# Kernel tuning notes

Measured on AMD Instinct MI355X. Metric: run time of the kernel, lower is better.

The kernel has to match this reference:

```python
import jax, jax.numpy as jnp
import numpy as np
from math import factorial, sqrt

BATCH = 4096
RS_IN = [(16, 0), (16, 1), (16, 2)]   # (mul, l), parity 0
RS_OUT = [(16, 0), (16, 1), (16, 2)]

# selection rule: l_filter in [|l_in-l_out|, l_in+l_out]
SET_LF = sorted({l for (_, li) in RS_IN for (_, lo) in RS_OUT
                 for l in range(abs(li - lo), li + lo + 1)})
Y_OFF = {l: sum(2 * k + 1 for k in SET_LF if k < l) for l in SET_LF}
Y_DIM = sum(2 * l + 1 for l in SET_LF)  # 25


def wigner_3j(j1, j2, j3, m1, m2, m3):
    if m1 + m2 + m3 != 0 or not (abs(j1 - j2) <= j3 <= j1 + j2):
        return 0.0
    if abs(m1) > j1 or abs(m2) > j2 or abs(m3) > j3:
        return 0.0
    f = factorial
    pre = sqrt(f(j1 + j2 - j3) * f(j1 - j2 + j3) * f(-j1 + j2 + j3) / f(j1 + j2 + j3 + 1))
    pre *= sqrt(f(j1 + m1) * f(j1 - m1) * f(j2 + m2) * f(j2 - m2) * f(j3 + m3) * f(j3 - m3))
    s = 0.0
    for t in range(max(0, j2 - j3 - m1, j1 - j3 + m2),
                   min(j1 + j2 - j3, j1 - m1, j2 + m2) + 1):
        s += (-1) ** t / (f(t) * f(j3 - j2 + m1 + t) * f(j3 - j1 - m2 + t)
                          * f(j1 + j2 - j3 - t) * f(j1 - m1 - t) * f(j2 + m2 - t))
    return (-1) ** (j1 - j2 - m3) * pre * s


def real_to_complex(l):
    # A[M+l, m+l]: complex Y^M expressed in the real SH basis
    A = np.zeros((2 * l + 1, 2 * l + 1), dtype=np.complex128)
    A[l, l] = 1.0
    s2 = 1.0 / np.sqrt(2.0)
    for m in range(1, l + 1):
        A[l + m, l + m] = (-1) ** m * s2
        A[l + m, l - m] = 1j * (-1) ** m * s2
        A[l - m, l + m] = s2
        A[l - m, l - m] = -1j * s2
    return A


def clebsch_gordan(l1, l2, l3):
    # real, unit-Frobenius-norm invariant 3-tensor (unique up to sign)
    T = np.zeros((2 * l1 + 1, 2 * l2 + 1, 2 * l3 + 1))
    for m1 in range(-l1, l1 + 1):
        for m2 in range(-l2, l2 + 1):
            m3 = -(m1 + m2)
            if abs(m3) <= l3:
                T[m1 + l1, m2 + l2, m3 + l3] = wigner_3j(l1, l2, l3, m1, m2, m3)
    A1, A2, A3 = real_to_complex(l1), real_to_complex(l2), real_to_complex(l3)
    C = np.einsum('abc,ai,bj,ck->ijk', T, A1.conj(), A2.conj(), A3.conj())
    C = C.real if np.linalg.norm(C.real) >= np.linalg.norm(C.imag) else C.imag
    n = np.linalg.norm(C)
    return (C / n).astype(np.float32) if n > 0 else C.astype(np.float32)


# precompute per-block padded CG tensors and R offsets
R_OFF = {}
C_BLOCKS = {}
_off = 0
for _i, (_mo, _lo) in enumerate(RS_OUT):
    for _j, (_mi, _li) in enumerate(RS_IN):
        _lfs = list(range(abs(_li - _lo), _li + _lo + 1))
        R_OFF[(_i, _j)] = (_off, len(_lfs))
        _off += _mo * _mi * len(_lfs)
        _C = np.zeros((len(_lfs), 2 * _lo + 1, 2 * _li + 1, Y_DIM), dtype=np.float32)
        for _k, _lf in enumerate(_lfs):
            _o = Y_OFF[_lf]
            _C[_k, :, :, _o:_o + 2 * _lf + 1] = clebsch_gordan(_lo, _li, _lf)
        C_BLOCKS[(_i, _j)] = jnp.asarray(_C)
N_PATH = _off  # 4864


def setup_inputs() -> dict:
    key = jax.random.key(0)
    k1, k2, k3 = jax.random.split(key, 3)
    Y = jax.random.normal(k1, (Y_DIM, BATCH), dtype=jnp.float32)
    R = jax.random.normal(k2, (BATCH, N_PATH), dtype=jnp.float32)
    norm_coef = jax.random.uniform(k3, (len(RS_OUT), len(RS_IN), BATCH),
                                   dtype=jnp.float32, minval=0.5, maxval=1.5)
    return {"Y": Y, "R": R, "norm_coef": norm_coef}


def reference(Y, R, norm_coef):
    # Y: [Y_DIM, batch], R: [batch, N_PATH], norm_coef: [3, 3, batch]
    batch = Y.shape[1]
    rows = []
    for i, (mo, lo) in enumerate(RS_OUT):
        row = []
        for j, (mi, li) in enumerate(RS_IN):
            off, nlf = R_OFF[(i, j)]
            sub_R = R[:, off:off + mo * mi * nlf].reshape(batch, mo, mi, nlf)
            # fuse the per-l_filter loop into one contraction over k and m
            K = jnp.einsum('kijm,mz,zuvk,z->zuivj',
                           C_BLOCKS[(i, j)], Y, sub_R, norm_coef[i, j])
            row.append(K.reshape(batch, mo * (2 * lo + 1), mi * (2 * li + 1)))
        rows.append(jnp.concatenate(row, axis=2))
    return jnp.concatenate(rows, axis=1)  # [batch, 144, 144]
```

## Files before the change

kernel.cpp:

```cpp
#include <hip/hip_runtime.h>

#define NPATH 4864
#define YDIM  25
#define NW    259
#define NCG   1225

__device__ float g_cg[NCG];
__device__ int   g_wtab[NW * 2];

__device__ __forceinline__ double dfact(int n) {
    double f = 1.0;
    for (int i = 2; i <= n; ++i) f *= (double)i;
    return f;
}
__device__ __forceinline__ int iabs_(int x) { return x < 0 ? -x : x; }
__device__ __forceinline__ int imax3(int a, int b, int c) { int m = a > b ? a : b; return m > c ? m : c; }
__device__ __forceinline__ int imin3(int a, int b, int c) { int m = a < b ? a : b; return m < c ? m : c; }

__device__ double wig3j(int j1, int j2, int j3, int m1, int m2, int m3) {
    if (m1 + m2 + m3 != 0) return 0.0;
    if (iabs_(m1) > j1 || iabs_(m2) > j2 || iabs_(m3) > j3) return 0.0;
    if (j3 < iabs_(j1 - j2) || j3 > j1 + j2) return 0.0;
    double pre = sqrt(dfact(j1 + j2 - j3) * dfact(j1 - j2 + j3) * dfact(-j1 + j2 + j3)
                      / dfact(j1 + j2 + j3 + 1));
    pre *= sqrt(dfact(j1 + m1) * dfact(j1 - m1) * dfact(j2 + m2) * dfact(j2 - m2)
                * dfact(j3 + m3) * dfact(j3 - m3));
    int t0 = imax3(0, j2 - j3 - m1, j1 - j3 + m2);
    int t1 = imin3(j1 + j2 - j3, j1 - m1, j2 + m2);
    double s = 0.0;
    for (int t = t0; t <= t1; ++t) {
        double d = dfact(t) * dfact(j3 - j2 + m1 + t) * dfact(j3 - j1 - m2 + t)
                 * dfact(j1 + j2 - j3 - t) * dfact(j1 - m1 - t) * dfact(j2 + m2 - t);
        s += ((t & 1) ? -1.0 : 1.0) / d;
    }
    int p = j1 - j2 - m3;
    p = ((p % 2) + 2) % 2;
    return (p ? -1.0 : 1.0) * pre * s;
}

__device__ void fill_A(int l, double* Are, double* Aim) {
    int n = 2 * l + 1;
    for (int i = 0; i < n * n; ++i) { Are[i] = 0.0; Aim[i] = 0.0; }
    Are[l * n + l] = 1.0;
    double s2 = sqrt(0.5);
    for (int m = 1; m <= l; ++m) {
        double sgn = (m & 1) ? -1.0 : 1.0;
        Are[(l + m) * n + (l + m)] = sgn * s2;
        Aim[(l + m) * n + (l - m)] = sgn * s2;
        Are[(l - m) * n + (l + m)] = s2;
        Aim[(l - m) * n + (l - m)] = -s2;
    }
}

__global__ __launch_bounds__(64) void setup_kernel() {
    const int CL1[19]  = {0,0,0,1,1,1,1,1,1,1,2,2,2,2,2,2,2,2,2};
    const int CL2[19]  = {0,1,2,0,1,1,1,2,2,2,0,1,1,1,2,2,2,2,2};
    const int CL3[19]  = {0,1,2,1,0,1,2,1,2,3,2,1,2,3,0,1,2,3,4};
    const int COFF[19] = {0,1,10,35,44,53,80,125,170,245,350,375,420,495,600,625,700,825,1000};

    int c = blockIdx.x;
    int t = threadIdx.x;

    if (c == 0 && t == 63) {
        const int NLFt[9]   = {1,1,1,1,3,3,1,3,5};
        const int CGOFF9[9] = {0,1,10,35,44,125,350,375,600};
        int w = 0;
        for (int ij = 0; ij < 9; ++ij) {
            int lo = ij / 3, li = ij % 3;
            int lfmin = lo > li ? lo - li : li - lo;
            int no2 = 2 * lo + 1, ni2 = 2 * li + 1;
            int cgo = CGOFF9[ij];
            for (int k = 0; k < NLFt[ij]; ++k) {
                int lf = lfmin + k;
                for (int a = 0; a < no2; ++a)
                    for (int b = 0; b < ni2; ++b) {
                        g_wtab[2 * w]     = cgo + (a * ni2 + b) * (2 * lf + 1);
                        g_wtab[2 * w + 1] = lf;
                        ++w;
                    }
                cgo += no2 * ni2 * (2 * lf + 1);
            }
        }
    }

    int l1 = CL1[c], l2 = CL2[c], l3 = CL3[c], coff = COFF[c];
    int n1 = 2 * l1 + 1, n2 = 2 * l2 + 1, n3 = 2 * l3 + 1;

    __shared__ double A1re[25], A1im[25], A2re[25], A2im[25], A3re[81], A3im[81];
    __shared__ double Tm[25];
    __shared__ double Cre[225], Cim[225];
    __shared__ double redR[64], redI[64];

    if (t == 0)      fill_A(l1, A1re, A1im);
    else if (t == 1) fill_A(l2, A2re, A2im);
    else if (t == 2) fill_A(l3, A3re, A3im);
    else if (t == 3) {
        for (int a = 0; a < n1; ++a)
            for (int b = 0; b < n2; ++b) {
                int m1 = a - l1, m2 = b - l2, m3 = -(m1 + m2);
                Tm[a * n2 + b] = (iabs_(m3) <= l3) ? wig3j(l1, l2, l3, m1, m2, m3) : 0.0;
            }
    }
    __syncthreads();

    int ntot = n1 * n2 * n3;
    double sre = 0.0, sim = 0.0;
    for (int idx = t; idx < ntot; idx += 64) {
        int i3 = idx % n3;
        int r  = idx / n3;
        int i2 = r % n2;
        int i1 = r / n2;
        double ar = 0.0, ai = 0.0;
        for (int a = 0; a < n1; ++a) {
            double x1r = A1re[a * n1 + i1], x1i = -A1im[a * n1 + i1];
            for (int b = 0; b < n2; ++b) {
                double tv = Tm[a * n2 + b];
                if (tv == 0.0) continue;
                int m3 = -((a - l1) + (b - l2));
                if (iabs_(m3) > l3) continue;
                double x2r = A2re[b * n2 + i2], x2i = -A2im[b * n2 + i2];
                double x3r = A3re[(m3 + l3) * n3 + i3], x3i = -A3im[(m3 + l3) * n3 + i3];
                double pr = x1r * x2r - x1i * x2i;
                double pi = x1r * x2i + x1i * x2r;
                double qr = pr * x3r - pi * x3i;
                double qi = pr * x3i + pi * x3r;
                ar += tv * qr;
                ai += tv * qi;
            }
        }
        Cre[idx] = ar; Cim[idx] = ai;
        sre += ar * ar; sim += ai * ai;
    }
    redR[t] = sre; redI[t] = sim;
    __syncthreads();
    if (t == 0) {
        double a = 0.0, b = 0.0;
        for (int q = 0; q < 64; ++q) { a += redR[q]; b += redI[q]; }
        redR[0] = a; redI[0] = b;
    }
    __syncthreads();
    double totR = redR[0], totI = redI[0];
    bool useRe = (totR >= totI);
    double nn  = sqrt(useRe ? totR : totI);
    double inv = (nn > 0.0) ? 1.0 / nn : 0.0;
    for (int idx = t; idx < ntot; idx += 64)
        g_cg[coff + idx] = (float)((useRe ? Cre[idx] : Cim[idx]) * inv);
}

template <int LO, int LI, int NLF_>
__device__ __forceinline__ void do_block(const float* __restrict__ Wl,
                                         const float* __restrict__ Rl,
                                         float nrm, float* __restrict__ outcol,
                                         int v, int b, int woff, int roff, int rowbase) {
    constexpr int NO2 = 2 * LO + 1, NI2 = 2 * LI + 1;
    float Wreg[NLF_ * NO2];
#pragma unroll
    for (int k = 0; k < NLF_; ++k)
#pragma unroll
        for (int a = 0; a < NO2; ++a)
            Wreg[k * NO2 + a] = Wl[woff + (k * NO2 + a) * NI2 + b];
#pragma unroll 4
    for (int u = 0; u < 16; ++u) {
        int rb = roff + (u * 16 + v) * NLF_;
        float Rk[NLF_];
#pragma unroll
        for (int k = 0; k < NLF_; ++k) Rk[k] = Rl[rb + k];
        float* orow = outcol + (rowbase + u * NO2) * 144;
#pragma unroll
        for (int a = 0; a < NO2; ++a) {
            float acc = 0.f;
#pragma unroll
            for (int k = 0; k < NLF_; ++k) acc += Wreg[k * NO2 + a] * Rk[k];
            orow[a * 144] = nrm * acc;
        }
    }
}

__global__ __launch_bounds__(256) void tp_kernel(const float* __restrict__ Yg,
                                                 const float* __restrict__ Rg,
                                                 const float* __restrict__ Ng,
                                                 float* __restrict__ Og, int batch) {
    __shared__ __align__(16) float Rl[NPATH];
    __shared__ float Wl[NW];
    __shared__ float Ys[YDIM];

    int z = blockIdx.x;
    int t = threadIdx.x;

    const float4* Rg4 = (const float4*)(Rg + (size_t)z * NPATH);
    float4* Rl4 = (float4*)Rl;
    for (int p = t; p < NPATH / 4; p += 256) Rl4[p] = Rg4[p];
    if (t < YDIM) Ys[t] = Yg[t * batch + z];
    __syncthreads();

    for (int w = t; w < NW; w += 256) {
        int off = g_wtab[2 * w], lf = g_wtab[2 * w + 1];
        float acc = 0.f;
        for (int ci = 0; ci <= 2 * lf; ++ci) acc += g_cg[off + ci] * Ys[lf * lf + ci];
        Wl[w] = acc;
    }
    __syncthreads();

    if (t >= 144) return;

    int j, v, b;
    if (t < 16)      { j = 0; v = t; b = 0; }
    else if (t < 64) { int q = t - 16; j = 1; v = q / 3; b = q - 3 * v; }
    else             { int q = t - 64; j = 2; v = q / 5; b = q - 5 * v; }

    float* outcol = Og + (size_t)z * 20736 + t;
    float n0 = Ng[(0 * 3 + j) * batch + z];
    float n1 = Ng[(1 * 3 + j) * batch + z];
    float n2 = Ng[(2 * 3 + j) * batch + z];

    if (j == 0) {
        do_block<0, 0, 1>(Wl, Rl, n0, outcol, v, b,   0,    0,  0);
        do_block<1, 0, 1>(Wl, Rl, n1, outcol, v, b,   9,  768, 16);
        do_block<2, 0, 1>(Wl, Rl, n2, outcol, v, b,  84, 2560, 64);
    } else if (j == 1) {
        do_block<0, 1, 1>(Wl, Rl, n0, outcol, v, b,   1,  256,  0);
        do_block<1, 1, 3>(Wl, Rl, n1, outcol, v, b,  12, 1024, 16);
        do_block<2, 1, 3>(Wl, Rl, n2, outcol, v, b,  89, 2816, 64);
    } else {
        do_block<0, 2, 1>(Wl, Rl, n0, outcol, v, b,   4,  512,  0);
        do_block<1, 2, 3>(Wl, Rl, n1, outcol, v, b,  39, 1792, 16);
        do_block<2, 2, 5>(Wl, Rl, n2, outcol, v, b, 134, 3584, 64);
    }
}

extern "C" void kernel_launch(void* const* d_in, const int* in_sizes, int n_in,
                              void* d_out, int out_size, void* d_ws, size_t ws_size,
                              hipStream_t stream) {
    const float* Y = (const float*)d_in[0];
    const float* R = (const float*)d_in[1];
    const float* N = (const float*)d_in[2];
    float* O = (float*)d_out;
    int batch = in_sizes[0] / YDIM;

    hipLaunchKernelGGL(setup_kernel, dim3(19), dim3(64), 0, stream);
    hipLaunchKernelGGL(tp_kernel, dim3(batch), dim3(256), 0, stream, Y, R, N, O, batch);
}
```

Baseline: 474.2 us.

## Precompute CG tables at compile time and align thread-to-column mapping to wavefronts

Moves Clebsch-Gordan coefficient and weight-offset table generation from a runtime setup kernel into constexpr evaluation stored in constant memory, which removes one kernel launch per call. It also remaps threads so each input-l group (j) starts on a 64-thread wavefront boundary, which avoids divergent branches inside a wavefront across the three do_block paths. The cost is more idle threads per block and reads from constant memory with non-uniform indices in the W computation.

```diff
diff --git a/kernel.cpp b/kernel.cpp
--- a/kernel.cpp
+++ b/kernel.cpp
@@ -5,147 +5,130 @@
 #define NW    259
 #define NCG   1225
 
-__device__ float g_cg[NCG];
-__device__ int   g_wtab[NW * 2];
-
-__device__ __forceinline__ double dfact(int n) {
-    double f = 1.0;
-    for (int i = 2; i <= n; ++i) f *= (double)i;
-    return f;
-}
-__device__ __forceinline__ int iabs_(int x) { return x < 0 ? -x : x; }
-__device__ __forceinline__ int imax3(int a, int b, int c) { int m = a > b ? a : b; return m > c ? m : c; }
-__device__ __forceinline__ int imin3(int a, int b, int c) { int m = a < b ? a : b; return m < c ? m : c; }
-
-__device__ double wig3j(int j1, int j2, int j3, int m1, int m2, int m3) {
+
+struct Tables {
+    float cg[NCG];
+    int   woff[NW];
+    int   wlf[NW];
+};
+
+constexpr double cfact(int n) { double f = 1.0; for (int i = 2; i <= n; ++i) f *= (double)i; return f; }
+
+constexpr double csqrt_(double x) {
+    if (x <= 0.0) return 0.0;
+    double g = x > 1.0 ? x : 1.0, p = 0.0;
+    for (int it = 0; it < 200; ++it) { p = g; g = 0.5 * (g + x / g); if (g == p) break; }
+    return g;
+}
+constexpr int cabs_(int x) { return x < 0 ? -x : x; }
+constexpr int cmax3(int a, int b, int c) { int m = a > b ? a : b; return m > c ? m : c; }
+constexpr int cmin3(int a, int b, int c) { int m = a < b ? a : b; return m < c ? m : c; }
+
+constexpr double cwig3j(int j1, int j2, int j3, int m1, int m2, int m3) {
     if (m1 + m2 + m3 != 0) return 0.0;
-    if (iabs_(m1) > j1 || iabs_(m2) > j2 || iabs_(m3) > j3) return 0.0;
-    if (j3 < iabs_(j1 - j2) || j3 > j1 + j2) return 0.0;
-    double pre = sqrt(dfact(j1 + j2 - j3) * dfact(j1 - j2 + j3) * dfact(-j1 + j2 + j3)
-                      / dfact(j1 + j2 + j3 + 1));
-    pre *= sqrt(dfact(j1 + m1) * dfact(j1 - m1) * dfact(j2 + m2) * dfact(j2 - m2)
-                * dfact(j3 + m3) * dfact(j3 - m3));
-    int t0 = imax3(0, j2 - j3 - m1, j1 - j3 + m2);
-    int t1 = imin3(j1 + j2 - j3, j1 - m1, j2 + m2);
+    if (cabs_(m1) > j1 || cabs_(m2) > j2 || cabs_(m3) > j3) return 0.0;
+    if (j3 < cabs_(j1 - j2) || j3 > j1 + j2) return 0.0;
+    double prod = cfact(j1 + j2 - j3) * cfact(j1 - j2 + j3) * cfact(-j1 + j2 + j3)
+                / cfact(j1 + j2 + j3 + 1);
+    prod *= cfact(j1 + m1) * cfact(j1 - m1) * cfact(j2 + m2) * cfact(j2 - m2)
+          * cfact(j3 + m3) * cfact(j3 - m3);
+    double pre = csqrt_(prod);
+    int t0 = cmax3(0, j2 - j3 - m1, j1 - j3 + m2);
+    int t1 = cmin3(j1 + j2 - j3, j1 - m1, j2 + m2);
     double s = 0.0;
     for (int t = t0; t <= t1; ++t) {
-        double d = dfact(t) * dfact(j3 - j2 + m1 + t) * dfact(j3 - j1 - m2 + t)
-                 * dfact(j1 + j2 - j3 - t) * dfact(j1 - m1 - t) * dfact(j2 + m2 - t);
+        double d = cfact(t) * cfact(j3 - j2 + m1 + t) * cfact(j3 - j1 - m2 + t)
+                 * cfact(j1 + j2 - j3 - t) * cfact(j1 - m1 - t) * cfact(j2 + m2 - t);
         s += ((t & 1) ? -1.0 : 1.0) / d;
     }
-    int p = j1 - j2 - m3;
-    p = ((p % 2) + 2) % 2;
+    int p = j1 - j2 - m3; p = ((p % 2) + 2) % 2;
     return (p ? -1.0 : 1.0) * pre * s;
 }
 
-__device__ void fill_A(int l, double* Are, double* Aim) {
-    int n = 2 * l + 1;
-    for (int i = 0; i < n * n; ++i) { Are[i] = 0.0; Aim[i] = 0.0; }
-    Are[l * n + l] = 1.0;
-    double s2 = sqrt(0.5);
-    for (int m = 1; m <= l; ++m) {
+struct Ent { int col; double re; double im; };
+
+constexpr int arow(int l, int a, Ent* e) {
+    int m = a - l;
+    double s2 = csqrt_(0.5);
+    if (m == 0) { e[0] = Ent{l, 1.0, 0.0}; return 1; }
+    if (m > 0) {
         double sgn = (m & 1) ? -1.0 : 1.0;
-        Are[(l + m) * n + (l + m)] = sgn * s2;
-        Aim[(l + m) * n + (l - m)] = sgn * s2;
-        Are[(l - m) * n + (l + m)] = s2;
-        Aim[(l - m) * n + (l - m)] = -s2;
-    }
-}
-
-__global__ __launch_bounds__(64) void setup_kernel() {
+        e[0] = Ent{l + m, sgn * s2, 0.0};
+        e[1] = Ent{l - m, 0.0, sgn * s2};
+        return 2;
+    }
+    int mm = -m;
+    e[0] = Ent{l + mm, s2, 0.0};
+    e[1] = Ent{l - mm, 0.0, -s2};
+    return 2;
+}
+
+constexpr Tables make_tables() {
+    Tables T{};
     const int CL1[19]  = {0,0,0,1,1,1,1,1,1,1,2,2,2,2,2,2,2,2,2};
     const int CL2[19]  = {0,1,2,0,1,1,1,2,2,2,0,1,1,1,2,2,2,2,2};
     const int CL3[19]  = {0,1,2,1,0,1,2,1,2,3,2,1,2,3,0,1,2,3,4};
     const int COFF[19] = {0,1,10,35,44,53,80,125,170,245,350,375,420,495,600,625,700,825,1000};
 
-    int c = blockIdx.x;
-    int t = threadIdx.x;
-
-    if (c == 0 && t == 63) {
-        const int NLFt[9]   = {1,1,1,1,3,3,1,3,5};
-        const int CGOFF9[9] = {0,1,10,35,44,125,350,375,600};
-        int w = 0;
-        for (int ij = 0; ij < 9; ++ij) {
-            int lo = ij / 3, li = ij % 3;
-            int lfmin = lo > li ? lo - li : li - lo;
-            int no2 = 2 * lo + 1, ni2 = 2 * li + 1;
-            int cgo = CGOFF9[ij];
-            for (int k = 0; k < NLFt[ij]; ++k) {
-                int lf = lfmin + k;
-                for (int a = 0; a < no2; ++a)
-                    for (int b = 0; b < ni2; ++b) {
-                        g_wtab[2 * w]     = cgo + (a * ni2 + b) * (2 * lf + 1);
-                        g_wtab[2 * w + 1] = lf;
-                        ++w;
-                    }
-                cgo += no2 * ni2 * (2 * lf + 1);
-            }
-        }
-    }
-
-    int l1 = CL1[c], l2 = CL2[c], l3 = CL3[c], coff = COFF[c];
-    int n1 = 2 * l1 + 1, n2 = 2 * l2 + 1, n3 = 2 * l3 + 1;
-
-    __shared__ double A1re[25], A1im[25], A2re[25], A2im[25], A3re[81], A3im[81];
-    __shared__ double Tm[25];
-    __shared__ double Cre[225], Cim[225];
-    __shared__ double redR[64], redI[64];
-
-    if (t == 0)      fill_A(l1, A1re, A1im);
-    else if (t == 1) fill_A(l2, A2re, A2im);
-    else if (t == 2) fill_A(l3, A3re, A3im);
-    else if (t == 3) {
+    for (int c = 0; c < 19; ++c) {
+        int l1 = CL1[c], l2 = CL2[c], l3 = CL3[c], coff = COFF[c];
+        int n1 = 2 * l1 + 1, n2 = 2 * l2 + 1, n3 = 2 * l3 + 1, ntot = n1 * n2 * n3;
+        double Cre[225] = {}, Cim[225] = {};
         for (int a = 0; a < n1; ++a)
             for (int b = 0; b < n2; ++b) {
                 int m1 = a - l1, m2 = b - l2, m3 = -(m1 + m2);
-                Tm[a * n2 + b] = (iabs_(m3) <= l3) ? wig3j(l1, l2, l3, m1, m2, m3) : 0.0;
+                if (cabs_(m3) > l3) continue;
+                double tv = cwig3j(l1, l2, l3, m1, m2, m3);
+                if (tv == 0.0) continue;
+                int crow = m3 + l3;
+                Ent e1[2] = {}, e2[2] = {}, e3[2] = {};
+                int k1 = arow(l1, a, e1), k2 = arow(l2, b, e2), k3 = arow(l3, crow, e3);
+                for (int x = 0; x < k1; ++x)
+                    for (int y = 0; y < k2; ++y)
+                        for (int w = 0; w < k3; ++w) {
+                            double r1 = e1[x].re, i1 = -e1[x].im;
+                            double r2 = e2[y].re, i2 = -e2[y].im;
+                            double r3 = e3[w].re, i3 = -e3[w].im;
+                            double pr = r1 * r2 - i1 * i2, pi = r1 * i2 + i1 * r2;
+                            double qr = pr * r3 - pi * i3, qi = pr * i3 + pi * r3;
+                            int idx = (e1[x].col * n2 + e2[y].col) * n3 + e3[w].col;
+                            Cre[idx] += tv * qr;
+                            Cim[idx] += tv * qi;
+                        }
             }
-    }
-    __syncthreads();
-
-    int ntot = n1 * n2 * n3;
-    double sre = 0.0, sim = 0.0;
-    for (int idx = t; idx < ntot; idx += 64) {
-        int i3 = idx % n3;
-        int r  = idx / n3;
-        int i2 = r % n2;
-        int i1 = r / n2;
-        double ar = 0.0, ai = 0.0;
-        for (int a = 0; a < n1; ++a) {
-            double x1r = A1re[a * n1 + i1], x1i = -A1im[a * n1 + i1];
-            for (int b = 0; b < n2; ++b) {
-                double tv = Tm[a * n2 + b];
-                if (tv == 0.0) continue;
-                int m3 = -((a - l1) + (b - l2));
-                if (iabs_(m3) > l3) continue;
-                double x2r = A2re[b * n2 + i2], x2i = -A2im[b * n2 + i2];
-                double x3r = A3re[(m3 + l3) * n3 + i3], x3i = -A3im[(m3 + l3) * n3 + i3];
-                double pr = x1r * x2r - x1i * x2i;
-                double pi = x1r * x2i + x1i * x2r;
-                double qr = pr * x3r - pi * x3i;
-                double qi = pr * x3i + pi * x3r;
-                ar += tv * qr;
-                ai += tv * qi;
-            }
+        double sR = 0.0, sI = 0.0;
+        for (int i = 0; i < ntot; ++i) { sR += Cre[i] * Cre[i]; sI += Cim[i] * Cim[i]; }
+        bool useRe = (sR >= sI);
+        double nn = csqrt_(useRe ? sR : sI);
+        double inv = nn > 0.0 ? 1.0 / nn : 0.0;
+        for (int i = 0; i < ntot; ++i)
+            T.cg[coff + i] = (float)((useRe ? Cre[i] : Cim[i]) * inv);
+    }
+
+    const int NLFt[9]   = {1,1,1,1,3,3,1,3,5};
+    const int CGOFF9[9] = {0,1,10,35,44,125,350,375,600};
+    int w = 0;
+    for (int ij = 0; ij < 9; ++ij) {
+        int lo = ij / 3, li = ij % 3;
+        int lfmin = lo > li ? lo - li : li - lo;
+        int no2 = 2 * lo + 1, ni2 = 2 * li + 1, cgo = CGOFF9[ij];
+        for (int k = 0; k < NLFt[ij]; ++k) {
+            int lf = lfmin + k;
+            for (int a = 0; a < no2; ++a)
+                for (int b = 0; b < ni2; ++b) {
+                    T.woff[w] = cgo + (a * ni2 + b) * (2 * lf + 1);
+                    T.wlf[w]  = lf;
+                    ++w;
+                }
+            cgo += no2 * ni2 * (2 * lf + 1);
         }
-        Cre[idx] = ar; Cim[idx] = ai;
-        sre += ar * ar; sim += ai * ai;
-    }
-    redR[t] = sre; redI[t] = sim;
-    __syncthreads();
-    if (t == 0) {
-        double a = 0.0, b = 0.0;
-        for (int q = 0; q < 64; ++q) { a += redR[q]; b += redI[q]; }
-        redR[0] = a; redI[0] = b;
-    }
-    __syncthreads();
-    double totR = redR[0], totI = redI[0];
-    bool useRe = (totR >= totI);
-    double nn  = sqrt(useRe ? totR : totI);
-    double inv = (nn > 0.0) ? 1.0 / nn : 0.0;
-    for (int idx = t; idx < ntot; idx += 64)
-        g_cg[coff + idx] = (float)((useRe ? Cre[idx] : Cim[idx]) * inv);
-}
+    }
+    return T;
+}
+
+constexpr Tables H_TAB = make_tables();
+__device__ __constant__ Tables d_tab = H_TAB;
+
 
 template <int LO, int LI, int NLF_>
 __device__ __forceinline__ void do_block(const float* __restrict__ Wl,
@@ -194,21 +177,20 @@
     __syncthreads();
 
     for (int w = t; w < NW; w += 256) {
-        int off = g_wtab[2 * w], lf = g_wtab[2 * w + 1];
+        int off = d_tab.woff[w], lf = d_tab.wlf[w];
         float acc = 0.f;
-        for (int ci = 0; ci <= 2 * lf; ++ci) acc += g_cg[off + ci] * Ys[lf * lf + ci];
+        for (int ci = 0; ci <= 2 * lf; ++ci) acc += d_tab.cg[off + ci] * Ys[lf * lf + ci];
         Wl[w] = acc;
     }
     __syncthreads();
 
-    if (t >= 144) return;
-
-    int j, v, b;
-    if (t < 16)      { j = 0; v = t; b = 0; }
-    else if (t < 64) { int q = t - 16; j = 1; v = q / 3; b = q - 3 * v; }
-    else             { int q = t - 64; j = 2; v = q / 5; b = q - 5 * v; }
-
-    float* outcol = Og + (size_t)z * 20736 + t;
+    int j, v, b, col;
+    if (t < 16)                     { j = 0; v = t; b = 0; col = t; }
+    else if (t >= 64 && t < 112)    { int q = t - 64;  j = 1; v = q / 3; b = q - 3 * v; col = 16 + q; }
+    else if (t >= 128 && t < 208)   { int q = t - 128; j = 2; v = q / 5; b = q - 5 * v; col = 64 + q; }
+    else return;
+
+    float* outcol = Og + (size_t)z * 20736 + col;
     float n0 = Ng[(0 * 3 + j) * batch + z];
     float n1 = Ng[(1 * 3 + j) * batch + z];
     float n2 = Ng[(2 * 3 + j) * batch + z];
@@ -237,6 +219,5 @@
     float* O = (float*)d_out;
     int batch = in_sizes[0] / YDIM;
 
-    hipLaunchKernelGGL(setup_kernel, dim3(19), dim3(64), 0, stream);
     hipLaunchKernelGGL(tp_kernel, dim3(batch), dim3(256), 0, stream, Y, R, N, O, batch);
 }
```

Result: faster. 420.2 us (-11.4%).
